# Kernel tuning notes

Measured on AMD Instinct MI355X. Metric: run time of the kernel, lower is better.

## Reference

```python
import jax, jax.numpy as jnp
import numpy as np

B, T, D = 2, 2048, 2048
H, HKV = 16, 16
SEM, GEO = 1024, 1024
DH = D // H          # 128, v head dim
DS = SEM // H        # 64, sem head dim
DG = GEO // H        # 64, geo head dim (== rope_dim)
ROPE_BASE = 10000.0


def _split_heads(x, n_heads, hd):
    b, t, _ = x.shape
    return x.reshape(b, t, n_heads, hd).transpose(0, 2, 1, 3)  # (B,H,T,hd)


def _rope(x, pos_offset):
    # x: (B,H,T,DG); rotate-half RoPE over the full geo head dim
    b, h, t, d = x.shape
    inv_freq = 1.0 / (ROPE_BASE ** (jnp.arange(0, d, 2, dtype=jnp.float32) / d))
    pos = jnp.arange(t, dtype=jnp.float32) + jnp.float32(pos_offset)
    ang = pos[:, None] * inv_freq[None, :]            # (T, d/2)
    cos, sin = jnp.cos(ang), jnp.sin(ang)             # (T, d/2)
    x1, x2 = x[..., : d // 2], x[..., d // 2 :]
    return jnp.concatenate([x1 * cos - x2 * sin, x2 * cos + x1 * sin], axis=-1)


def setup_inputs() -> dict:
    key = jax.random.key(0)
    ks = jax.random.split(key, 8)
    s = lambda fan_in: 1.0 / np.sqrt(fan_in)
    return {
        "x": jax.random.normal(ks[0], (B, T, D), dtype=jnp.float32),
        "Wq_sem": jax.random.normal(ks[1], (D, SEM), dtype=jnp.float32) * s(D),
        "Wk_sem": jax.random.normal(ks[2], (D, SEM), dtype=jnp.float32) * s(D),
        "Wq_geo": jax.random.normal(ks[3], (D, GEO), dtype=jnp.float32) * s(D),
        "Wk_geo": jax.random.normal(ks[4], (D, GEO), dtype=jnp.float32) * s(D),
        "Wv": jax.random.normal(ks[5], (D, D), dtype=jnp.float32) * s(D),
        "Wo": jax.random.normal(ks[6], (D, D), dtype=jnp.float32) * s(D),
        "gate_logit": jax.random.normal(ks[7], (H,), dtype=jnp.float32) * 0.1,
        "pos_offset": 0,
    }


def reference(x, Wq_sem, Wk_sem, Wq_geo, Wk_geo, Wv, Wo, gate_logit, pos_offset):
    qsh = _split_heads(x @ Wq_sem, H, DS)    # (B,H,T,DS)
    ksh = _split_heads(x @ Wk_sem, HKV, DS)
    qgh = _split_heads(x @ Wq_geo, H, DG)    # (B,H,T,DG)
    kgh = _split_heads(x @ Wk_geo, HKV, DG)
    vh = _split_heads(x @ Wv, HKV, DH)       # (B,H,T,DH)

    qgh = _rope(qgh, pos_offset)
    kgh = _rope(kgh, pos_offset)

    gate = jax.nn.sigmoid(gate_logit).reshape(1, H, 1, 1).astype(x.dtype)
    qsh = qsh * (2.0 * gate)
    qgh = qgh * (2.0 - 2.0 * gate)

    sem_scale = 1.0 / np.sqrt(float(DS))
    geo_scale = 1.0 / np.sqrt(float(DG))
    # decoupled logits: sem and geo contributions each with their own scale
    logits = (jnp.einsum("bhqd,bhkd->bhqk", qsh, ksh) * sem_scale
              + jnp.einsum("bhqd,bhkd->bhqk", qgh, kgh) * geo_scale)

    t = x.shape[1]
    causal = jnp.tril(jnp.ones((t, t), dtype=bool))
    logits = jnp.where(causal, logits, jnp.finfo(logits.dtype).min)
    attn = jax.nn.softmax(logits, axis=-1)

    out_h = jnp.einsum("bhqk,bhkd->bhqd", attn, vh)   # (B,H,T,DH)
    out = out_h.transpose(0, 2, 1, 3).reshape(x.shape[0], t, H * DH)
    return out @ Wo
```

## Files before the change

kernel.cpp:

```cpp
#include <hip/hip_runtime.h>
#include <hip/hip_bf16.h>
#include <math.h>

#define B_ 2
#define T_ 2048
#define D_ 2048
#define H_ 16
#define DH_ 128
#define SEM_ 1024
#define GEO_ 1024
#define NPROJ 6144

typedef unsigned short ushort_t;
typedef short bf16x8 __attribute__((ext_vector_type(8)));
typedef float f32x4 __attribute__((ext_vector_type(4)));

static __device__ inline ushort_t f2b(float x) {
    __hip_bfloat16 h = __float2bfloat16(x);
    return *reinterpret_cast<ushort_t*>(&h);
}
static __device__ inline float b2f(ushort_t u) {
    union { unsigned int i; float f; } v; v.i = ((unsigned int)u) << 16; return v.f;
}
static __device__ inline void gload_lds16(const ushort_t* g, ushort_t* l) {
    __builtin_amdgcn_global_load_lds(
        (const __attribute__((address_space(1))) void*)g,
        (__attribute__((address_space(3))) void*)l, 16, 0, 0);
}

__global__ __launch_bounds__(256) void convert_x(
    const float* __restrict__ x, ushort_t* __restrict__ xh)
{
    size_t i = ((size_t)blockIdx.x * 256 + threadIdx.x) * 8;
    float4 a = *(const float4*)&x[i];
    float4 b = *(const float4*)&x[i + 4];
    bf16x8 o;
    o[0] = (short)f2b(a.x); o[1] = (short)f2b(a.y);
    o[2] = (short)f2b(a.z); o[3] = (short)f2b(a.w);
    o[4] = (short)f2b(b.x); o[5] = (short)f2b(b.y);
    o[6] = (short)f2b(b.z); o[7] = (short)f2b(b.w);
    *(bf16x8*)&xh[i] = o;
}

__global__ __launch_bounds__(256) void transpose_all(
    const float* __restrict__ W0, const float* __restrict__ W1,
    const float* __restrict__ W2, const float* __restrict__ W3,
    const float* __restrict__ W4, const float* __restrict__ W5,
    ushort_t* __restrict__ Wt_all, ushort_t* __restrict__ WoT)
{
    const int z = blockIdx.z;
    const float* W;
    ushort_t* dst;
    int N;
    switch (z) {
        case 0: W = W0; dst = Wt_all;                          N = 1024; break;
        case 1: W = W1; dst = Wt_all + (size_t)1024 * 2048;    N = 1024; break;
        case 2: W = W2; dst = Wt_all + (size_t)2048 * 2048;    N = 1024; break;
        case 3: W = W3; dst = Wt_all + (size_t)3072 * 2048;    N = 1024; break;
        case 4: W = W4; dst = Wt_all + (size_t)4096 * 2048;    N = 2048; break;
        default: W = W5; dst = WoT;                            N = 2048; break;
    }
    const int n0 = blockIdx.x * 32;
    if (n0 >= N) return;
    const int k0 = blockIdx.y * 32;

    __shared__ float tile[32][33];
    const int c = threadIdx.x & 31, r = threadIdx.x >> 5;
#pragma unroll
    for (int rr = 0; rr < 32; rr += 8)
        tile[r + rr][c] = W[(size_t)(k0 + r + rr) * N + n0 + c];
    __syncthreads();
#pragma unroll
    for (int rr = 0; rr < 32; rr += 8)
        dst[(size_t)(n0 + r + rr) * 2048 + k0 + c] = f2b(tile[c][r + rr]);
}

#define BARS()  { asm volatile("" ::: "memory"); __builtin_amdgcn_s_barrier(); asm volatile("" ::: "memory"); }
#define WL0()   asm volatile("s_waitcnt lgkmcnt(0)" ::: "memory")
#define WV6()   asm volatile("s_waitcnt vmcnt(6)" ::: "memory")

#define LDA8(par, iq, i4, kk) \
    (*(const bf16x8*)&smA[(par)*16384 + (iq)*8192 + aoff + (i4)*1024 + ((kk) ? ca1 : ca0)])
#define LDB8(par, jq, j1, kk) \
    (*(const bf16x8*)&smB[(par)*16384 + (jq)*8192 + boff + (j1)*2048 + ((kk) ? ca1 : ca0)])

#define READ_A(par, iq) \
    aF[0]=LDA8(par,iq,0,0); aF[1]=LDA8(par,iq,0,1); \
    aF[2]=LDA8(par,iq,1,0); aF[3]=LDA8(par,iq,1,1); \
    aF[4]=LDA8(par,iq,2,0); aF[5]=LDA8(par,iq,2,1); \
    aF[6]=LDA8(par,iq,3,0); aF[7]=LDA8(par,iq,3,1);

#define READ_B(par, jq) \
    bF[(jq)*4+0]=LDB8(par,jq,0,0); bF[(jq)*4+1]=LDB8(par,jq,0,1); \
    bF[(jq)*4+2]=LDB8(par,jq,1,0); bF[(jq)*4+3]=LDB8(par,jq,1,1);

#define STAGE_A(h, kt, par) do { \
    const ushort_t* _s = gAbase + (size_t)((h)*128) * 2048 + (kt)*64 + stgoff; \
    ushort_t* _d = smA + (par)*16384 + (h)*8192 + wid*512; \
    gload_lds16(_s, _d); \
    gload_lds16(_s + (size_t)64*2048, _d + 4096); \
} while(0)

#define STAGE_B(h, kt, par) do { \
    const ushort_t* _s = gBbase + (size_t)((h)*128) * 2048 + (kt)*64 + stgoff; \
    ushort_t* _d = smB + (par)*16384 + (h)*8192 + wid*512; \
    gload_lds16(_s, _d); \
    gload_lds16(_s + (size_t)64*2048, _d + 4096); \
} while(0)

#define MM16(iq, jq) do { \
    _Pragma("unroll") \
    for (int i4 = 0; i4 < 4; ++i4) { \
        acc[(iq)*4+i4][(jq)*2+0] = __builtin_amdgcn_mfma_f32_16x16x32_bf16(aF[i4*2+0], bF[(jq)*4+0], acc[(iq)*4+i4][(jq)*2+0], 0, 0, 0); \
        acc[(iq)*4+i4][(jq)*2+0] = __builtin_amdgcn_mfma_f32_16x16x32_bf16(aF[i4*2+1], bF[(jq)*4+1], acc[(iq)*4+i4][(jq)*2+0], 0, 0, 0); \
        acc[(iq)*4+i4][(jq)*2+1] = __builtin_amdgcn_mfma_f32_16x16x32_bf16(aF[i4*2+0], bF[(jq)*4+2], acc[(iq)*4+i4][(jq)*2+1], 0, 0, 0); \
        acc[(iq)*4+i4][(jq)*2+1] = __builtin_amdgcn_mfma_f32_16x16x32_bf16(aF[i4*2+1], bF[(jq)*4+3], acc[(iq)*4+i4][(jq)*2+1], 0, 0, 0); \
    } \
} while(0)

#define TILE_BODY(par, parn, kt1, kt2) \
    READ_A(par, 0); READ_B(par, 0); STAGE_A(1, kt1, parn); \
    BARS(); WL0(); \
    __builtin_amdgcn_s_setprio(1); MM16(0, 0); __builtin_amdgcn_s_setprio(0); \
    BARS(); \
    READ_B(par, 1); STAGE_A(0, kt2, par); \
    BARS(); WL0(); \
    __builtin_amdgcn_s_setprio(1); MM16(0, 1); __builtin_amdgcn_s_setprio(0); \
    BARS(); \
    READ_A(par, 1); STAGE_B(0, kt2, par); \
    BARS(); WL0(); \
    __builtin_amdgcn_s_setprio(1); MM16(1, 1); __builtin_amdgcn_s_setprio(0); \
    BARS(); \
    STAGE_B(1, kt2, par); WV6(); \
    BARS(); \
    __builtin_amdgcn_s_setprio(1); MM16(1, 0); __builtin_amdgcn_s_setprio(0); \
    BARS();

__global__ __launch_bounds__(512, 2) void gemm_proj(
    const ushort_t* __restrict__ A, const ushort_t* __restrict__ Bt,
    const float* __restrict__ gate_logit, const int* __restrict__ pos_off,
    ushort_t* __restrict__ Qh, ushort_t* __restrict__ Kh,
    ushort_t* __restrict__ Vt)
{
    extern __shared__ __align__(16) ushort_t smdyn[];
    ushort_t* smA = smdyn;
    ushort_t* smB = smdyn + 32768;

    const int tid  = threadIdx.x;
    const int wid  = tid >> 6, lane = tid & 63;
    const int ln16 = lane & 15, g = lane >> 4;
    const int wm = wid & 1, wn = wid >> 1;
    const int m0 = blockIdx.y * 256, n0 = blockIdx.x * 256;

    const int srow = wid * 8 + (lane >> 3);
    const int scol = ((lane & 7) ^ (lane >> 3)) * 8;
    const size_t stgoff = (size_t)srow * 2048 + scol;
    const ushort_t* gAbase = A  + (size_t)m0 * 2048;
    const ushort_t* gBbase = Bt + (size_t)n0 * 2048;

    const int cg0 = ln16 & 7;
    const int ca0 = ((g + 0) ^ cg0) * 8;
    const int ca1 = ((g + 4) ^ cg0) * 8;
    const int aoff = wm * 4096 + ln16 * 64;
    const int boff = (wn >> 1) * 4096 + (wn & 1) * 1024 + ln16 * 64;

    f32x4 acc[8][4];
#pragma unroll
    for (int i = 0; i < 8; ++i)
#pragma unroll
        for (int j = 0; j < 4; ++j) acc[i][j] = (f32x4){0.f, 0.f, 0.f, 0.f};
    bf16x8 aF[8], bF[8];

    STAGE_A(0, 0, 0); STAGE_B(0, 0, 0); STAGE_B(1, 0, 0); STAGE_A(1, 0, 0);
    STAGE_A(0, 1, 1); STAGE_B(0, 1, 1); STAGE_B(1, 1, 1);
    WV6();
    BARS();

#pragma unroll 1
    for (int t = 0; t < 32; t += 2) {
        const int ka1 = t + 1;
        const int ka2 = (t + 2 < 32) ? t + 2 : 31;
        const int kb1 = ka2;
        const int kb2 = (t + 3 < 32) ? t + 3 : 31;
        TILE_BODY(0, 1, ka1, ka2);
        TILE_BODY(1, 0, kb1, kb2);
    }
    asm volatile("s_waitcnt vmcnt(0)" ::: "memory");

    const int region = n0 >> 10;
    const int rbase  = m0 + wm * 64 + g * 4;

    if (region <= 1) {
        ushort_t* dst = (region == 0) ? Qh : Kh;
        const int hb  = ((n0 & 1023) >> 6) + (wn >> 1);
        const int d64 = (wn & 1) * 16 + ln16;
        float sc0 = 1.0f, sc1 = 1.0f;
        if (region == 0) {
            sc0 = 0.25f / (1.0f + __expf(-gate_logit[hb]));
            sc1 = 0.25f / (1.0f + __expf(-gate_logit[hb + 2]));
        }
#pragma unroll
        for (int i = 0; i < 8; ++i)
#pragma unroll
            for (int r = 0; r < 4; ++r) {
                int row = rbase + (i >> 2) * 128 + (i & 3) * 16 + r;
                int t = row & (T_ - 1), bb = row >> 11;
                size_t b0 = ((size_t)(bb * H_ + hb)     * T_ + t) * 128;
                size_t b1 = ((size_t)(bb * H_ + hb + 2) * T_ + t) * 128;
                dst[b0 + d64]      = f2b(acc[i][0][r] * sc0);
                dst[b0 + d64 + 32] = f2b(acc[i][1][r] * sc0);
                dst[b1 + d64]      = f2b(acc[i][2][r] * sc1);
                dst[b1 + d64 + 32] = f2b(acc[i][3][r] * sc1);
            }
    } else if (region <= 3) {
        ushort_t* dst = (region == 2) ? Qh : Kh;
        const int hb = ((n0 & 1023) >> 6) + (wn >> 1);
        const int ip = (wn & 1) * 16 + ln16;
        const float invf = __expf(-0.28782313665087625f * (float)ip);
        const float po = (float)(*pos_off);
        float sc0 = 1.0f, sc1 = 1.0f;
        if (region == 2) {
            sc0 = 0.25f * (1.0f - 1.0f / (1.0f + __expf(-gate_logit[hb])));
            sc1 = 0.25f * (1.0f - 1.0f / (1.0f + __expf(-gate_logit[hb + 2])));
        }
#pragma unroll
        for (int i = 0; i < 8; ++i)
#pragma unroll
            for (int r = 0; r < 4; ++r) {
                int row = rbase + (i >> 2) * 128 + (i & 3) * 16 + r;
                int t = row & (T_ - 1), bb = row >> 11;
                float s, c;
                __sincosf(((float)t + po) * invf, &s, &c);
                size_t b0 = ((size_t)(bb * H_ + hb)     * T_ + t) * 128;
                size_t b1 = ((size_t)(bb * H_ + hb + 2) * T_ + t) * 128;
                float x1 = acc[i][0][r], x2 = acc[i][1][r];
                dst[b0 + 64 + ip] = f2b((x1 * c - x2 * s) * sc0);
                dst[b0 + 96 + ip] = f2b((x2 * c + x1 * s) * sc0);
                x1 = acc[i][2][r]; x2 = acc[i][3][r];
                dst[b1 + 64 + ip] = f2b((x1 * c - x2 * s) * sc1);
                dst[b1 + 96 + ip] = f2b((x2 * c + x1 * s) * sc1);
            }
    } else {
        const int hb = (n0 - 4096) >> 7;
        const int db = (wn >> 1) * 64 + (wn & 1) * 16 + ln16;
#pragma unroll
        for (int i = 0; i < 8; ++i)
#pragma unroll
            for (int r = 0; r < 4; ++r) {
                int row = rbase + (i >> 2) * 128 + (i & 3) * 16 + r;
                int t = row & (T_ - 1), bb = row >> 11;
                size_t v0 = ((size_t)(bb * H_ + hb)     * DH_ + db) * T_ + t;
                size_t v1 = ((size_t)(bb * H_ + hb + 1) * DH_ + db) * T_ + t;
                Vt[v0]                    = f2b(acc[i][0][r]);
                Vt[v0 + (size_t)32 * T_]  = f2b(acc[i][1][r]);
                Vt[v1]                    = f2b(acc[i][2][r]);
                Vt[v1 + (size_t)32 * T_]  = f2b(acc[i][3][r]);
            }
    }
}

__global__ __launch_bounds__(256) void gemm_bt_f32(
    const ushort_t* __restrict__ A, const ushort_t* __restrict__ Bt,
    float* __restrict__ C, int M, int N, int K)
{
    __shared__ ushort_t As[128 * 32];
    __shared__ ushort_t Bs[128 * 32];

    const int tid  = threadIdx.x;
    const int wid  = tid >> 6, lane = tid & 63;
    const int ln16 = lane & 15, g = lane >> 4;
    const int wm = wid & 1, wn = wid >> 1;
    const int m0 = blockIdx.y * 128, n0 = blockIdx.x * 128;

    const int lrow = lane >> 2;
    const int lc8  = (lane & 3) * 8;
    const ushort_t* gA = A  + (size_t)(m0 + wid * 32 + lrow) * K + lc8;
    const ushort_t* gB = Bt + (size_t)(n0 + wid * 32 + lrow) * K + lc8;
    ushort_t* lA = As + wid * 1024;
    ushort_t* lB = Bs + wid * 1024;
    const size_t K16 = (size_t)16 * K;

    f32x4 acc[4][4];
#pragma unroll
    for (int i = 0; i < 4; ++i)
#pragma unroll
        for (int j = 0; j < 4; ++j) acc[i][j] = (f32x4){0.f, 0.f, 0.f, 0.f};

    for (int k0 = 0; k0 < K; k0 += 32) {
        __syncthreads();
        gload_lds16(gA,       lA);
        gload_lds16(gA + K16, lA + 512);
        gload_lds16(gB,       lB);
        gload_lds16(gB + K16, lB + 512);
        gA += 32; gB += 32;
        __syncthreads();

        bf16x8 af[4], bfr[4];
#pragma unroll
        for (int i = 0; i < 4; ++i)
            af[i] = *(const bf16x8*)&As[(wm * 64 + i * 16 + ln16) * 32 + g * 8];
#pragma unroll
        for (int j = 0; j < 4; ++j)
            bfr[j] = *(const bf16x8*)&Bs[(wn * 64 + j * 16 + ln16) * 32 + g * 8];
#pragma unroll
        for (int i = 0; i < 4; ++i)
#pragma unroll
            for (int j = 0; j < 4; ++j)
                acc[i][j] = __builtin_amdgcn_mfma_f32_16x16x32_bf16(
                    af[i], bfr[j], acc[i][j], 0, 0, 0);
    }

#pragma unroll
    for (int i = 0; i < 4; ++i)
#pragma unroll
        for (int j = 0; j < 4; ++j)
#pragma unroll
            for (int r = 0; r < 4; ++r) {
                int row = m0 + wm * 64 + i * 16 + g * 4 + r;
                int col = n0 + wn * 64 + j * 16 + ln16;
                C[(size_t)row * N + col] = acc[i][j][r];
            }
}

#define P_PITCH  40

__global__ __launch_bounds__(256) void flash_attn(
    const ushort_t* __restrict__ Qh,
    const ushort_t* __restrict__ Kh,
    const ushort_t* __restrict__ Vt,
    ushort_t* __restrict__ aoh)
{
    __shared__ ushort_t Ks[32 * 128];
    __shared__ ushort_t Vs[128 * 32];
    __shared__ ushort_t Pl[4 * 16 * P_PITCH];

    const int tid  = threadIdx.x;
    const int wid  = tid >> 6, lane = tid & 63;
    const int ln16 = lane & 15, g = lane >> 4;
    const int p    = blockIdx.x;
    const int h  = blockIdx.y, b = blockIdx.z;
    const int bh = b * H_ + h;

    const ushort_t* Kbase = Kh + (size_t)bh * T_ * 128;
    const ushort_t* Vbase = Vt + (size_t)bh * 128 * T_;
    ushort_t* Pw = Pl + wid * 16 * P_PITCH;

    const int sk0 = tid,      sk1 = 256 + tid;
    const int kr0 = sk0 >> 4, kc0 = sk0 & 15;
    const int kr1 = sk1 >> 4, kc1 = sk1 & 15;
    const int vd0 = sk0 >> 2, vg0 = sk0 & 3;
    const int vd1 = sk1 >> 2, vg1 = sk1 & 3;
    const int kofs0 = (kc0 ^ (kr0 & 15)) * 8, kofs1 = (kc1 ^ (kr1 & 15)) * 8;
    const int vofs0 = (vg0 ^ ((vd0 + (vd0 >> 2)) & 3)) * 8;
    const int vofs1 = (vg1 ^ ((vd1 + (vd1 >> 2)) & 3)) * 8;

    bf16x8 bones;
    {
        short o = (ln16 == 0) ? (short)0x3F80 : (short)0;
#pragma unroll
        for (int j = 0; j < 8; ++j) bones[j] = o;
    }

#pragma unroll 1
    for (int ti = 0; ti < 2; ++ti) {
        const int qt = ti ? (31 - p) : p;
        const int q0 = qt * 64;
        const int qw = q0 + wid * 16;

        bf16x8 aq[4];
        {
            const ushort_t* qrow = Qh + ((size_t)bh * T_ + qw + ln16) * 128;
#pragma unroll
            for (int c2 = 0; c2 < 4; ++c2)
                aq[c2] = *(const bf16x8*)(qrow + c2 * 32 + g * 8);
        }

        f32x4 acc[8];
#pragma unroll
        for (int i = 0; i < 8; ++i) acc[i] = (f32x4){0.f, 0.f, 0.f, 0.f};
        f32x4 acc_l = (f32x4){0.f, 0.f, 0.f, 0.f};

        const int nkb  = q0 / 32 + 2;
        const int qmax = qw + 15;

        for (int kb = 0; kb < nkb; ++kb) {
            const int kt = kb * 32;
            __syncthreads();
            gload_lds16(Kbase + (size_t)(kt + kr0) * 128 + kofs0, Ks + wid * 512);
            gload_lds16(Kbase + (size_t)(kt + kr1) * 128 + kofs1, Ks + 2048 + wid * 512);
            gload_lds16(Vbase + (size_t)vd0 * T_ + kt + vofs0,    Vs + wid * 512);
            gload_lds16(Vbase + (size_t)vd1 * T_ + kt + vofs1,    Vs + 2048 + wid * 512);
            __syncthreads();
            if (kt > qmax) continue;

            f32x4 s0 = (f32x4){0.f, 0.f, 0.f, 0.f};
            f32x4 s1 = (f32x4){0.f, 0.f, 0.f, 0.f};
#pragma unroll
            for (int c2 = 0; c2 < 4; ++c2) {
                int jk = c2 * 4 + g;
                bf16x8 bk0 = *(const bf16x8*)&Ks[(ln16 * 16 + (jk ^ ln16)) * 8];
                bf16x8 bk1 = *(const bf16x8*)&Ks[(256 + ln16 * 16 + (jk ^ ln16)) * 8];
                s0 = __builtin_amdgcn_mfma_f32_16x16x32_bf16(aq[c2], bk0, s0, 0, 0, 0);
                s1 = __builtin_amdgcn_mfma_f32_16x16x32_bf16(aq[c2], bk1, s1, 0, 0, 0);
            }

            const bool diag = (kt + 31 > qw);
#pragma unroll
            for (int r2 = 0; r2 < 4; ++r2) {
                float e0 = __expf(s0[r2] - 12.0f);
                float e1 = __expf(s1[r2] - 12.0f);
                if (diag) {
                    int qr = qw + g * 4 + r2;
                    e0 = (kt + ln16      > qr) ? 0.0f : e0;
                    e1 = (kt + 16 + ln16 > qr) ? 0.0f : e1;
                }
                int prow = g * 4 + r2;
                Pw[prow * P_PITCH + ln16]      = f2b(e0);
                Pw[prow * P_PITCH + 16 + ln16] = f2b(e1);
            }
            __asm__ volatile("s_waitcnt lgkmcnt(0)" ::: "memory");
            bf16x8 ap = *(const bf16x8*)&Pw[ln16 * P_PITCH + g * 8];

#pragma unroll
            for (int cdv = 0; cdv < 8; ++cdv) {
                int d = cdv * 16 + ln16;
                bf16x8 bv = *(const bf16x8*)
                    &Vs[((d << 2) + (g ^ ((d + (d >> 2)) & 3))) * 8];
                acc[cdv] = __builtin_amdgcn_mfma_f32_16x16x32_bf16(ap, bv, acc[cdv], 0, 0, 0);
            }
            acc_l = __builtin_amdgcn_mfma_f32_16x16x32_bf16(ap, bones, acc_l, 0, 0, 0);
        }

        float invl[4];
#pragma unroll
        for (int r2 = 0; r2 < 4; ++r2)
            invl[r2] = 1.0f / __shfl(acc_l[r2], lane & 48);
#pragma unroll
        for (int cdv = 0; cdv < 8; ++cdv)
#pragma unroll
            for (int r2 = 0; r2 < 4; ++r2) {
                int qr = qw + g * 4 + r2;
                aoh[((size_t)b * T_ + qr) * D_ + h * DH_ + cdv * 16 + ln16] =
                    f2b(acc[cdv][r2] * invl[r2]);
            }
    }
}

extern "C" void kernel_launch(void* const* d_in, const int* in_sizes, int n_in,
                              void* d_out, int out_size, void* d_ws, size_t ws_size,
                              hipStream_t stream)
{
    const float* x       = (const float*)d_in[0];
    const float* Wq_sem  = (const float*)d_in[1];
    const float* Wk_sem  = (const float*)d_in[2];
    const float* Wq_geo  = (const float*)d_in[3];
    const float* Wk_geo  = (const float*)d_in[4];
    const float* Wv      = (const float*)d_in[5];
    const float* Wo      = (const float*)d_in[6];
    const float* gate    = (const float*)d_in[7];
    const int*   pos_off = (const int*)d_in[8];
    float* out = (float*)d_out;

    const int M = B_ * T_;
    char* ws = (char*)d_ws;
    ushort_t* xh     = (ushort_t*)(ws);
    ushort_t* aoh    = xh;
    ushort_t* Wt_all = (ushort_t*)(ws + (size_t)16 * 1048576);
    ushort_t* WoT    = (ushort_t*)(ws + (size_t)40 * 1048576);
    ushort_t* Qh     = (ushort_t*)(ws + (size_t)48 * 1048576);
    ushort_t* Kh     = (ushort_t*)(ws + (size_t)64 * 1048576);
    ushort_t* Vt     = (ushort_t*)(ws + (size_t)80 * 1048576);

    dim3 blk(256);

    convert_x<<<(M * D_) / (256 * 8), blk, 0, stream>>>(x, xh);
    transpose_all<<<dim3(64, 64, 6), blk, 0, stream>>>(
        Wq_sem, Wk_sem, Wq_geo, Wk_geo, Wv, Wo, Wt_all, WoT);

    hipFuncSetAttribute((const void*)gemm_proj,
                        hipFuncAttributeMaxDynamicSharedMemorySize, 131072);
    gemm_proj<<<dim3(NPROJ / 256, M / 256), dim3(512), 131072, stream>>>(
        xh, Wt_all, gate, pos_off, Qh, Kh, Vt);

    flash_attn<<<dim3(16, H_, B_), blk, 0, stream>>>(Qh, Kh, Vt, aoh);

    gemm_bt_f32<<<dim3(D_ / 128, M / 128), blk, 0, stream>>>(
        aoh, WoT, out, M, D_, D_);
}
```

Before: 423.5 us.

## Prefetch next-tile LDS fragments early, swizzle block order, vectorize V stores

Moves the LDS fragment reads so each one is issued right after the preceding MFMA group, and reads the next tile's first A/B fragments at the end of the current tile. This lets LDS read latency overlap with matrix math instead of stalling before each MFMA group. It also remaps the block index with a grouped swizzle to improve L2 reuse across neighbouring blocks, and packs the transposed V epilogue writes into 4-element vector stores. The extra in-flight fragments may raise register pressure, and the final wait now also drains LDS counters.

```diff
diff --git a/kernel.cpp b/kernel.cpp
--- a/kernel.cpp
+++ b/kernel.cpp
@@ -14,6 +14,7 @@
 typedef unsigned short ushort_t;
 typedef short bf16x8 __attribute__((ext_vector_type(8)));
 typedef float f32x4 __attribute__((ext_vector_type(4)));
+typedef unsigned short us4 __attribute__((ext_vector_type(4)));
 
 static __device__ inline ushort_t f2b(float x) {
     __hip_bfloat16 h = __float2bfloat16(x);
@@ -119,21 +120,24 @@
 } while(0)
 
 #define TILE_BODY(par, parn, kt1, kt2) \
-    READ_A(par, 0); READ_B(par, 0); STAGE_A(1, kt1, parn); \
+    STAGE_A(1, kt1, parn); \
     BARS(); WL0(); \
     __builtin_amdgcn_s_setprio(1); MM16(0, 0); __builtin_amdgcn_s_setprio(0); \
+    READ_B(par, 1); \
     BARS(); \
-    READ_B(par, 1); STAGE_A(0, kt2, par); \
+    STAGE_A(0, kt2, par); \
     BARS(); WL0(); \
     __builtin_amdgcn_s_setprio(1); MM16(0, 1); __builtin_amdgcn_s_setprio(0); \
+    READ_A(par, 1); \
     BARS(); \
-    READ_A(par, 1); STAGE_B(0, kt2, par); \
+    STAGE_B(0, kt2, par); \
     BARS(); WL0(); \
     __builtin_amdgcn_s_setprio(1); MM16(1, 1); __builtin_amdgcn_s_setprio(0); \
     BARS(); \
     STAGE_B(1, kt2, par); WV6(); \
     BARS(); \
     __builtin_amdgcn_s_setprio(1); MM16(1, 0); __builtin_amdgcn_s_setprio(0); \
+    READ_A(parn, 0); READ_B(parn, 0); \
     BARS();
 
 __global__ __launch_bounds__(512, 2) void gemm_proj(
@@ -150,7 +154,10 @@
     const int wid  = tid >> 6, lane = tid & 63;
     const int ln16 = lane & 15, g = lane >> 4;
     const int wm = wid & 1, wn = wid >> 1;
-    const int m0 = blockIdx.y * 256, n0 = blockIdx.x * 256;
+
+    const int lin = blockIdx.y * 24 + blockIdx.x;
+    const int swz = (lin & 7) * 48 + (lin >> 3);
+    const int m0 = (swz / 24) * 256, n0 = (swz % 24) * 256;
 
     const int srow = wid * 8 + (lane >> 3);
     const int scol = ((lane & 7) ^ (lane >> 3)) * 8;
@@ -175,6 +182,7 @@
     STAGE_A(0, 1, 1); STAGE_B(0, 1, 1); STAGE_B(1, 1, 1);
     WV6();
     BARS();
+    READ_A(0, 0); READ_B(0, 0);
 
 #pragma unroll 1
     for (int t = 0; t < 32; t += 2) {
@@ -185,7 +193,7 @@
         TILE_BODY(0, 1, ka1, ka2);
         TILE_BODY(1, 0, kb1, kb2);
     }
-    asm volatile("s_waitcnt vmcnt(0)" ::: "memory");
+    asm volatile("s_waitcnt vmcnt(0) lgkmcnt(0)" ::: "memory");
 
     const int region = n0 >> 10;
     const int rbase  = m0 + wm * 64 + g * 4;
@@ -244,18 +252,19 @@
         const int hb = (n0 - 4096) >> 7;
         const int db = (wn >> 1) * 64 + (wn & 1) * 16 + ln16;
 #pragma unroll
-        for (int i = 0; i < 8; ++i)
-#pragma unroll
-            for (int r = 0; r < 4; ++r) {
-                int row = rbase + (i >> 2) * 128 + (i & 3) * 16 + r;
-                int t = row & (T_ - 1), bb = row >> 11;
-                size_t v0 = ((size_t)(bb * H_ + hb)     * DH_ + db) * T_ + t;
-                size_t v1 = ((size_t)(bb * H_ + hb + 1) * DH_ + db) * T_ + t;
-                Vt[v0]                    = f2b(acc[i][0][r]);
-                Vt[v0 + (size_t)32 * T_]  = f2b(acc[i][1][r]);
-                Vt[v1]                    = f2b(acc[i][2][r]);
-                Vt[v1 + (size_t)32 * T_]  = f2b(acc[i][3][r]);
-            }
+        for (int i = 0; i < 8; ++i) {
+            int row0 = rbase + (i >> 2) * 128 + (i & 3) * 16;
+            int t0 = row0 & (T_ - 1), bb = row0 >> 11;
+#pragma unroll
+            for (int j = 0; j < 4; ++j) {
+                us4 v;
+                v[0] = f2b(acc[i][j][0]); v[1] = f2b(acc[i][j][1]);
+                v[2] = f2b(acc[i][j][2]); v[3] = f2b(acc[i][j][3]);
+                int hh = hb + (j >> 1);
+                int dd = db + (j & 1) * 32;
+                *(us4*)&Vt[((size_t)(bb * H_ + hh) * DH_ + dd) * T_ + t0] = v;
+            }
+        }
     }
 }
 
```

New measurement: 397.9 us. 1.06x faster.
